# Kernel optimization log

Measured on AMD Instinct MI355X. Metric: run time of the kernel, lower is better.

Reference implementation:

```python
import jax, jax.numpy as jnp
import numpy as np

B, N, F_IN, F_OUT = 8, 2048, 512, 512


def setup_inputs() -> dict:
    key = jax.random.key(0)
    k1, k2, k3, k4 = jax.random.split(key, 4)
    X = jax.random.normal(k1, (B, N, F_IN), dtype=jnp.float32)
    A = jax.random.uniform(k2, (B, N, N), dtype=jnp.float32)
    # nn.Linear params (kaiming-uniform-ish scale is irrelevant for correctness)
    bound = 1.0 / np.sqrt(F_IN)
    W = jax.random.uniform(k3, (F_IN, F_OUT), dtype=jnp.float32, minval=-bound, maxval=bound)
    b = jax.random.uniform(k4, (F_OUT,), dtype=jnp.float32, minval=-bound, maxval=bound)
    return {"X": X, "A": A, "W": W, "b": b}


def reference(X, A, W, b):
    # A' = A + I  (self-loops)
    A_hat = A + jnp.eye(A.shape[-1], dtype=A.dtype)
    # D^{-1/2}: per-row degree of A'.  torch builds diag_embed + two bmms;
    # mathematically identical to broadcasted row/column scaling.
    d_inv_sqrt = A_hat.sum(axis=-1) ** -0.5                      # [B, N]
    L = A_hat * d_inv_sqrt[:, :, None] * d_inv_sqrt[:, None, :]  # [B, N, N]
    x = X @ W + b                                                # [B, N, F_out]
    return jnp.einsum('bij,bjf->bif', L, x)
```

## Files before the change

### kernel.cpp

```cpp
#include <hip/hip_runtime.h>

#define B_ 8
#define N_ 2048
#define FIN_ 512
#define FOUT_ 512

typedef __attribute__((ext_vector_type(8))) short short8;
typedef __attribute__((ext_vector_type(4))) float floatx4;
typedef __attribute__((ext_vector_type(4))) unsigned short ushortx4;
typedef __attribute__((ext_vector_type(8))) unsigned short ushortx8;

__device__ inline unsigned short f2bf(float f) {
    union { float f; unsigned int u; } x; x.f = f;
    unsigned int r = x.u + 0x7FFFu + ((x.u >> 16) & 1u);
    return (unsigned short)(r >> 16);
}

__device__ inline void glds16(const void* g, void* l) {
    __builtin_amdgcn_global_load_lds(
        (const __attribute__((address_space(1))) void*)g,
        (__attribute__((address_space(3))) void*)l, 16, 0, 0);
}

__global__ __launch_bounds__(256) void prep_kernel(
    const float* __restrict__ A, float* __restrict__ dinv,
    unsigned short* __restrict__ Abf,
    const float* __restrict__ X, unsigned short* __restrict__ Xbf,
    const float* __restrict__ W, unsigned short* __restrict__ Wt) {
    int t = threadIdx.x;
    int bid = blockIdx.x;

    {
        size_t e0 = ((size_t)bid * 256 + t) * 8;
        float4 a0 = *(const float4*)(X + e0);
        float4 a1 = *(const float4*)(X + e0 + 4);
        float av[8] = {a0.x, a0.y, a0.z, a0.w, a1.x, a1.y, a1.z, a1.w};
        ushortx8 p;
#pragma unroll
        for (int r = 0; r < 8; ++r) p[r] = f2bf(av[r]);
        *(ushortx8*)(Xbf + e0) = p;
    }

    __shared__ float tile[32][33];
    if (bid < 256) {
        int bx = (bid & 15) * 32;
        int by = (bid >> 4) * 32;
        int tx = t & 31, ty = t >> 5;
#pragma unroll
        for (int r = 0; r < 32; r += 8)
            tile[ty + r][tx] = W[(size_t)(by + ty + r) * FOUT_ + bx + tx];
        __syncthreads();
#pragma unroll
        for (int r = 0; r < 32; r += 8)
            Wt[(size_t)(bx + ty + r) * FIN_ + by + tx] = f2bf(tile[tx][ty + r]);
    }

    int lane = t & 63;
    int row = bid * 4 + (t >> 6);
    size_t base = (size_t)row * N_;
    const float4* A4 = (const float4*)(A + base);
    float4 v[8];
#pragma unroll
    for (int c = 0; c < 8; ++c) v[c] = A4[c * 64 + lane];
    float s = 0.f;
#pragma unroll
    for (int c = 0; c < 8; ++c) {
        ushortx4 p;
        p[0] = f2bf(v[c].x); p[1] = f2bf(v[c].y);
        p[2] = f2bf(v[c].z); p[3] = f2bf(v[c].w);
        *(ushortx4*)(Abf + base + (size_t)(c * 64 + lane) * 4) = p;
        s += v[c].x + v[c].y + v[c].z + v[c].w;
    }
#pragma unroll
    for (int off = 32; off > 0; off >>= 1) s += __shfl_down(s, off, 64);
    if (lane == 0) dinv[row] = rsqrtf(s + 1.0f);
}


__global__ __launch_bounds__(256) void gemm1_kernel(
    const unsigned short* __restrict__ Abase,
    const unsigned short* __restrict__ Btbase,
    unsigned short* __restrict__ XwT,
    const float* __restrict__ bias,
    const float* __restrict__ dinv) {
    __shared__ __align__(16) char smem[65536];

    int t = threadIdx.x;
    int lane = t & 63;
    int wave = t >> 6;
    int wr = wave >> 1, wc = wave & 1;
    int q = lane >> 4, m = lane & 15;
    int n0 = blockIdx.x * 128;
    int m0 = blockIdx.y * 128;

    int srow = t >> 3;
    int scol = (((t & 7) ^ (srow & 7)) * 8);
    int x0 = ((q ^ (m & 7)) * 16);
    int x1 = x0 ^ 64;

    floatx4 acc[4][4];
#pragma unroll
    for (int mi = 0; mi < 4; ++mi)
#pragma unroll
        for (int ni = 0; ni < 4; ++ni)
            acc[mi][ni] = (floatx4){0.f, 0.f, 0.f, 0.f};

    const unsigned short* gA = Abase + (size_t)(m0 + srow) * FIN_ + scol;
    const unsigned short* gB = Btbase + (size_t)(n0 + srow) * FIN_ + scol;

#define STAGE1(bufi) do {                                              \
        char* lA = smem + (bufi) * 32768 + wave * 1024;                \
        char* lB = smem + (bufi) * 32768 + 16384 + wave * 1024;        \
        _Pragma("unroll")                                              \
        for (int u = 0; u < 4; ++u) {                                  \
            glds16(gA + (size_t)(u * 32) * FIN_, lA + u * 4096);       \
            glds16(gB + (size_t)(u * 32) * FIN_, lB + u * 4096);       \
        }                                                              \
        gA += 64; gB += 64;                                            \
    } while (0)

    STAGE1(0);
    STAGE1(1);

    const int NT = FIN_ / 64;
    for (int kt = 0; kt < NT; ++kt) {
        if (kt < NT - 1) asm volatile("s_waitcnt vmcnt(8)" ::: "memory");
        else             asm volatile("s_waitcnt vmcnt(0)" ::: "memory");
        __builtin_amdgcn_sched_barrier(0);
        __builtin_amdgcn_s_barrier();
        const char* As = smem + (kt & 1) * 32768;
        const char* Bs = As + 16384;
        short8 af0[4], bf0[4], af1[4], bf1[4];
#pragma unroll
        for (int mi = 0; mi < 4; ++mi)
            af0[mi] = *(const short8*)(As + (wr * 64 + mi * 16 + m) * 128 + x0);
#pragma unroll
        for (int ni = 0; ni < 4; ++ni)
            bf0[ni] = *(const short8*)(Bs + (wc * 64 + ni * 16 + m) * 128 + x0);
#pragma unroll
        for (int mi = 0; mi < 4; ++mi)
            af1[mi] = *(const short8*)(As + (wr * 64 + mi * 16 + m) * 128 + x1);
#pragma unroll
        for (int ni = 0; ni < 4; ++ni)
            bf1[ni] = *(const short8*)(Bs + (wc * 64 + ni * 16 + m) * 128 + x1);
        asm volatile("s_waitcnt lgkmcnt(8)" ::: "memory");
        __builtin_amdgcn_sched_barrier(0);
        __builtin_amdgcn_s_setprio(1);
#pragma unroll
        for (int mi = 0; mi < 4; ++mi)
#pragma unroll
            for (int ni = 0; ni < 4; ++ni)
                acc[mi][ni] = __builtin_amdgcn_mfma_f32_16x16x32_bf16(
                    af0[mi], bf0[ni], acc[mi][ni], 0, 0, 0);
        __builtin_amdgcn_s_setprio(0);
        asm volatile("s_waitcnt lgkmcnt(0)" ::: "memory");
        __builtin_amdgcn_sched_barrier(0);
        __builtin_amdgcn_s_barrier();
        if (kt + 2 < NT) STAGE1(kt & 1);
        __builtin_amdgcn_sched_barrier(0);
        __builtin_amdgcn_s_setprio(1);
#pragma unroll
        for (int mi = 0; mi < 4; ++mi)
#pragma unroll
            for (int ni = 0; ni < 4; ++ni)
                acc[mi][ni] = __builtin_amdgcn_mfma_f32_16x16x32_bf16(
                    af1[mi], bf1[ni], acc[mi][ni], 0, 0, 0);
        __builtin_amdgcn_s_setprio(0);
    }
#undef STAGE1

    unsigned short* T = (unsigned short*)smem;
#pragma unroll
    for (int mi = 0; mi < 4; ++mi) {
        int row = wr * 64 + mi * 16 + q * 4;
        float4 dv = *(const float4*)(dinv + m0 + row);
        float dr[4] = {dv.x, dv.y, dv.z, dv.w};
#pragma unroll
        for (int ni = 0; ni < 4; ++ni) {
            int col = wc * 64 + ni * 16 + m;
            float bv = bias[n0 + col];
            ushortx4 pk;
#pragma unroll
            for (int r = 0; r < 4; ++r) pk[r] = f2bf((acc[mi][ni][r] + bv) * dr[r]);
            *(ushortx4*)(T + col * 136 + row) = pk;
        }
    }
    __syncthreads();
    int f  = t >> 1;
    int c0 = (t & 1) * 64;
    int bb = m0 >> 11;
    int node0 = (m0 & 2047) + c0;
    unsigned short* dst = XwT + ((size_t)bb * FOUT_ + n0 + f) * N_ + node0;
    const unsigned short* src = T + f * 136 + c0;
#pragma unroll
    for (int u = 0; u < 8; ++u)
        *(ushortx8*)(dst + u * 8) = *(const ushortx8*)(src + u * 8);
}

__global__ __launch_bounds__(256) void gemm2_kernel(
    const unsigned short* __restrict__ Abf,
    const unsigned short* __restrict__ XwT,
    const float* __restrict__ dinv,
    float* __restrict__ out) {
    __shared__ __align__(16) char smem[65536];

    int t = threadIdx.x;
    int lane = t & 63;
    int wave = t >> 6;
    int wr = wave >> 1, wc = wave & 1;
    int q = lane >> 4, m = lane & 15;

    int id = blockIdx.x;
    int b  = id & 7;
    int s  = id >> 3;
    int n0 = (s & 3) * 128;
    int m0 = (s >> 2) * 128;

    const unsigned short* Ab = Abf + (size_t)b * N_ * N_;
    const unsigned short* Bb = XwT + (size_t)b * FOUT_ * N_;

    int srow = t >> 3;
    int scol = (((t & 7) ^ (srow & 7)) * 8);
    int x0 = ((q ^ (m & 7)) * 16);
    int x1 = x0 ^ 64;

    floatx4 acc[4][4];
#pragma unroll
    for (int mi = 0; mi < 4; ++mi)
#pragma unroll
        for (int ni = 0; ni < 4; ++ni)
            acc[mi][ni] = (floatx4){0.f, 0.f, 0.f, 0.f};

    const unsigned short* gA = Ab + (size_t)(m0 + srow) * N_ + scol;
    const unsigned short* gB = Bb + (size_t)(n0 + srow) * N_ + scol;

#define STAGE2(bufi) do {                                              \
        char* lA = smem + (bufi) * 32768 + wave * 1024;                \
        char* lB = smem + (bufi) * 32768 + 16384 + wave * 1024;        \
        _Pragma("unroll")                                              \
        for (int u = 0; u < 4; ++u) {                                  \
            glds16(gA + (size_t)(u * 32) * N_, lA + u * 4096);         \
            glds16(gB + (size_t)(u * 32) * N_, lB + u * 4096);         \
        }                                                              \
        gA += 64; gB += 64;                                            \
    } while (0)

    STAGE2(0);
    STAGE2(1);

    const int NT = N_ / 64;
    for (int kt = 0; kt < NT; ++kt) {
        if (kt < NT - 1) asm volatile("s_waitcnt vmcnt(8)" ::: "memory");
        else             asm volatile("s_waitcnt vmcnt(0)" ::: "memory");
        __builtin_amdgcn_sched_barrier(0);
        __builtin_amdgcn_s_barrier();
        const char* As = smem + (kt & 1) * 32768;
        const char* Bs = As + 16384;
        short8 af0[4], bf0[4], af1[4], bf1[4];
#pragma unroll
        for (int mi = 0; mi < 4; ++mi)
            af0[mi] = *(const short8*)(As + (wr * 64 + mi * 16 + m) * 128 + x0);
#pragma unroll
        for (int ni = 0; ni < 4; ++ni)
            bf0[ni] = *(const short8*)(Bs + (wc * 64 + ni * 16 + m) * 128 + x0);
#pragma unroll
        for (int mi = 0; mi < 4; ++mi)
            af1[mi] = *(const short8*)(As + (wr * 64 + mi * 16 + m) * 128 + x1);
#pragma unroll
        for (int ni = 0; ni < 4; ++ni)
            bf1[ni] = *(const short8*)(Bs + (wc * 64 + ni * 16 + m) * 128 + x1);
        asm volatile("s_waitcnt lgkmcnt(8)" ::: "memory");
        __builtin_amdgcn_sched_barrier(0);
        __builtin_amdgcn_s_setprio(1);
#pragma unroll
        for (int mi = 0; mi < 4; ++mi)
#pragma unroll
            for (int ni = 0; ni < 4; ++ni)
                acc[mi][ni] = __builtin_amdgcn_mfma_f32_16x16x32_bf16(
                    af0[mi], bf0[ni], acc[mi][ni], 0, 0, 0);
        __builtin_amdgcn_s_setprio(0);
        asm volatile("s_waitcnt lgkmcnt(0)" ::: "memory");
        __builtin_amdgcn_sched_barrier(0);
        __builtin_amdgcn_s_barrier();
        if (kt + 2 < NT) STAGE2(kt & 1);
        __builtin_amdgcn_sched_barrier(0);
        __builtin_amdgcn_s_setprio(1);
#pragma unroll
        for (int mi = 0; mi < 4; ++mi)
#pragma unroll
            for (int ni = 0; ni < 4; ++ni)
                acc[mi][ni] = __builtin_amdgcn_mfma_f32_16x16x32_bf16(
                    af1[mi], bf1[ni], acc[mi][ni], 0, 0, 0);
        __builtin_amdgcn_s_setprio(0);
    }
#undef STAGE2

    float* C = out + (size_t)b * N_ * FOUT_;
#pragma unroll
    for (int mi = 0; mi < 4; ++mi) {
        int rowb = m0 + wr * 64 + mi * 16 + q * 4;
        float4 dv = *(const float4*)(dinv + b * N_ + rowb);
        float dr[4] = {dv.x, dv.y, dv.z, dv.w};
#pragma unroll
        for (int ni = 0; ni < 4; ++ni) {
            int col = n0 + wc * 64 + ni * 16 + m;
            ushortx4 yv = *(const ushortx4*)(Bb + (size_t)col * N_ + rowb);
#pragma unroll
            for (int r = 0; r < 4; ++r) {
                union { unsigned int u; float f; } yc; yc.u = ((unsigned int)yv[r]) << 16;
                C[(size_t)(rowb + r) * FOUT_ + col] = dr[r] * (acc[mi][ni][r] + yc.f);
            }
        }
    }
}

extern "C" void kernel_launch(void* const* d_in, const int* in_sizes, int n_in,
                              void* d_out, int out_size, void* d_ws, size_t ws_size,
                              hipStream_t stream) {
    const float* X    = (const float*)d_in[0];
    const float* A    = (const float*)d_in[1];
    const float* W    = (const float*)d_in[2];
    const float* bias = (const float*)d_in[3];
    float* out = (float*)d_out;
    char* ws = (char*)d_ws;

    float* dinv          = (float*)(ws);
    unsigned short* Xbf  = (unsigned short*)(ws + (1u << 16));
    unsigned short* Wt   = (unsigned short*)(ws + (1u << 16) + 16777216u);
    unsigned short* XwT  = (unsigned short*)(ws + (1u << 16) + 16777216u + 524288u);
    unsigned short* Abf  = (unsigned short*)(ws + (1u << 16) + 16777216u + 524288u + 16777216u);

    prep_kernel<<<B_ * N_ / 4, 256, 0, stream>>>(A, dinv, Abf, X, Xbf, W, Wt);

    gemm1_kernel<<<dim3(FOUT_ / 128, (B_ * N_) / 128), 256, 0, stream>>>(
        Xbf, Wt, XwT, bias, dinv);

    gemm2_kernel<<<512, 256, 0, stream>>>(Abf, XwT, dinv, out);
}
```

Before: 283.1 us.

## Restructure prep kernel into grid-stride A conversion with atomic row-sum accumulation

The prep kernel is reorganized so 2048 blocks stream-convert A to bf16 in 256-element chunks with a grid-stride loop. Partial row sums are accumulated via atomic adds into a zeroed buffer. The separate 512 blocks handle the W transpose and X conversion. The rsqrt of the degree is moved into the GEMM epilogues. This changes the work distribution and memory access pattern of the bandwidth-bound prep stage, at the cost of an extra memset launch, many atomics, and nondeterministic float summation order.

Result: slower. 305.6 us (+7.9%).

```diff
diff --git a/kernel.cpp b/kernel.cpp
--- a/kernel.cpp
+++ b/kernel.cpp
@@ -23,57 +23,57 @@
 }
 
 __global__ __launch_bounds__(256) void prep_kernel(
-    const float* __restrict__ A, float* __restrict__ dinv,
+    const float* __restrict__ A, float* __restrict__ dsum,
     unsigned short* __restrict__ Abf,
     const float* __restrict__ X, unsigned short* __restrict__ Xbf,
     const float* __restrict__ W, unsigned short* __restrict__ Wt) {
     int t = threadIdx.x;
     int bid = blockIdx.x;
-
-    {
-        size_t e0 = ((size_t)bid * 256 + t) * 8;
-        float4 a0 = *(const float4*)(X + e0);
-        float4 a1 = *(const float4*)(X + e0 + 4);
-        float av[8] = {a0.x, a0.y, a0.z, a0.w, a1.x, a1.y, a1.z, a1.w};
-        ushortx8 p;
-#pragma unroll
-        for (int r = 0; r < 8; ++r) p[r] = f2bf(av[r]);
-        *(ushortx8*)(Xbf + e0) = p;
-    }
-
     __shared__ float tile[32][33];
-    if (bid < 256) {
-        int bx = (bid & 15) * 32;
-        int by = (bid >> 4) * 32;
-        int tx = t & 31, ty = t >> 5;
-#pragma unroll
-        for (int r = 0; r < 32; r += 8)
-            tile[ty + r][tx] = W[(size_t)(by + ty + r) * FOUT_ + bx + tx];
-        __syncthreads();
-#pragma unroll
-        for (int r = 0; r < 32; r += 8)
-            Wt[(size_t)(bx + ty + r) * FIN_ + by + tx] = f2bf(tile[tx][ty + r]);
-    }
-
-    int lane = t & 63;
-    int row = bid * 4 + (t >> 6);
-    size_t base = (size_t)row * N_;
-    const float4* A4 = (const float4*)(A + base);
-    float4 v[8];
-#pragma unroll
-    for (int c = 0; c < 8; ++c) v[c] = A4[c * 64 + lane];
-    float s = 0.f;
-#pragma unroll
-    for (int c = 0; c < 8; ++c) {
-        ushortx4 p;
-        p[0] = f2bf(v[c].x); p[1] = f2bf(v[c].y);
-        p[2] = f2bf(v[c].z); p[3] = f2bf(v[c].w);
-        *(ushortx4*)(Abf + base + (size_t)(c * 64 + lane) * 4) = p;
-        s += v[c].x + v[c].y + v[c].z + v[c].w;
-    }
-#pragma unroll
-    for (int off = 32; off > 0; off >>= 1) s += __shfl_down(s, off, 64);
-    if (lane == 0) dinv[row] = rsqrtf(s + 1.0f);
+
+    if (bid < 2048) {
+        int lane = t & 63;
+        int gw = bid * 4 + (t >> 6);
+        const int NCHUNK = (B_ * N_ * N_) / 256;
+#pragma unroll 2
+        for (int c = gw; c < NCHUNK; c += 8192) {
+            size_t e = (size_t)c * 256 + lane * 4;
+            float4 v = *(const float4*)(A + e);
+            ushortx4 p;
+            p[0] = f2bf(v.x); p[1] = f2bf(v.y);
+            p[2] = f2bf(v.z); p[3] = f2bf(v.w);
+            *(ushortx4*)(Abf + e) = p;
+            float s = v.x + v.y + v.z + v.w;
+#pragma unroll
+            for (int off = 32; off > 0; off >>= 1) s += __shfl_down(s, off, 64);
+            if (lane == 0) unsafeAtomicAdd(dsum + (c >> 3), s);
+        }
+    } else {
+        int xb = bid - 2048;
+        if (xb < 256) {
+            int bx = (xb & 15) * 32;
+            int by = (xb >> 4) * 32;
+            int tx = t & 31, ty = t >> 5;
+#pragma unroll
+            for (int r = 0; r < 32; r += 8)
+                tile[ty + r][tx] = W[(size_t)(by + ty + r) * FOUT_ + bx + tx];
+            __syncthreads();
+#pragma unroll
+            for (int r = 0; r < 32; r += 8)
+                Wt[(size_t)(bx + ty + r) * FIN_ + by + tx] = f2bf(tile[tx][ty + r]);
+        }
+        const size_t NG = ((size_t)B_ * N_ * FIN_) / 8;
+        for (size_t g = (size_t)xb * 256 + t; g < NG; g += 512 * 256) {
+            size_t e0 = g * 8;
+            float4 a0 = *(const float4*)(X + e0);
+            float4 a1 = *(const float4*)(X + e0 + 4);
+            float av[8] = {a0.x, a0.y, a0.z, a0.w, a1.x, a1.y, a1.z, a1.w};
+            ushortx8 p;
+#pragma unroll
+            for (int r = 0; r < 8; ++r) p[r] = f2bf(av[r]);
+            *(ushortx8*)(Xbf + e0) = p;
+        }
+    }
 }
 
 
@@ -82,7 +82,7 @@
     const unsigned short* __restrict__ Btbase,
     unsigned short* __restrict__ XwT,
     const float* __restrict__ bias,
-    const float* __restrict__ dinv) {
+    const float* __restrict__ dsum) {
     __shared__ __align__(16) char smem[65536];
 
     int t = threadIdx.x;
@@ -173,8 +173,9 @@
 #pragma unroll
     for (int mi = 0; mi < 4; ++mi) {
         int row = wr * 64 + mi * 16 + q * 4;
-        float4 dv = *(const float4*)(dinv + m0 + row);
-        float dr[4] = {dv.x, dv.y, dv.z, dv.w};
+        float4 dv = *(const float4*)(dsum + m0 + row);
+        float dr[4] = {rsqrtf(dv.x + 1.f), rsqrtf(dv.y + 1.f),
+                       rsqrtf(dv.z + 1.f), rsqrtf(dv.w + 1.f)};
 #pragma unroll
         for (int ni = 0; ni < 4; ++ni) {
             int col = wc * 64 + ni * 16 + m;
@@ -200,7 +201,7 @@
 __global__ __launch_bounds__(256) void gemm2_kernel(
     const unsigned short* __restrict__ Abf,
     const unsigned short* __restrict__ XwT,
-    const float* __restrict__ dinv,
+    const float* __restrict__ dsum,
     float* __restrict__ out) {
     __shared__ __align__(16) char smem[65536];
 
@@ -299,8 +300,9 @@
 #pragma unroll
     for (int mi = 0; mi < 4; ++mi) {
         int rowb = m0 + wr * 64 + mi * 16 + q * 4;
-        float4 dv = *(const float4*)(dinv + b * N_ + rowb);
-        float dr[4] = {dv.x, dv.y, dv.z, dv.w};
+        float4 dv = *(const float4*)(dsum + b * N_ + rowb);
+        float dr[4] = {rsqrtf(dv.x + 1.f), rsqrtf(dv.y + 1.f),
+                       rsqrtf(dv.z + 1.f), rsqrtf(dv.w + 1.f)};
 #pragma unroll
         for (int ni = 0; ni < 4; ++ni) {
             int col = n0 + wc * 64 + ni * 16 + m;
@@ -324,16 +326,18 @@
     float* out = (float*)d_out;
     char* ws = (char*)d_ws;
 
-    float* dinv          = (float*)(ws);
+    float* dsum          = (float*)(ws);
     unsigned short* Xbf  = (unsigned short*)(ws + (1u << 16));
     unsigned short* Wt   = (unsigned short*)(ws + (1u << 16) + 16777216u);
     unsigned short* XwT  = (unsigned short*)(ws + (1u << 16) + 16777216u + 524288u);
     unsigned short* Abf  = (unsigned short*)(ws + (1u << 16) + 16777216u + 524288u + 16777216u);
 
-    prep_kernel<<<B_ * N_ / 4, 256, 0, stream>>>(A, dinv, Abf, X, Xbf, W, Wt);
+    hipMemsetAsync(dsum, 0, (size_t)B_ * N_ * sizeof(float), stream);
+
+    prep_kernel<<<2560, 256, 0, stream>>>(A, dsum, Abf, X, Xbf, W, Wt);
 
     gemm1_kernel<<<dim3(FOUT_ / 128, (B_ * N_) / 128), 256, 0, stream>>>(
-        Xbf, Wt, XwT, bias, dinv);
-
-    gemm2_kernel<<<512, 256, 0, stream>>>(Abf, XwT, dinv, out);
-}
+        Xbf, Wt, XwT, bias, dsum);
+
+    gemm2_kernel<<<512, 256, 0, stream>>>(Abf, XwT, dsum, out);
+}
```
